# Optimization experiments

Measured on AMD Instinct MI355X. Metric: run time of the kernel, lower is better.

## Reference

```python
import jax, jax.numpy as jnp
import numpy as np

B = 8192
D = 512          # encode_length
H = 1024         # projection hidden
S = 4096         # fine_Nums (fine prototypes)
Y = 256          # coarse_num
GUMBEL_TEMP = 0.5
EPS_LOG = 1e-9
EPS_GUMBEL = 1e-20


def setup_inputs() -> dict:
    key = jax.random.key(0)
    ks = jax.random.split(key, 16)
    g = lambda k, shape, s: jax.random.normal(k, shape, dtype=jnp.float32) * s
    glorot = lambda k, shape: jax.random.uniform(k, shape, dtype=jnp.float32,
                                                 minval=-1.0, maxval=1.0) * jnp.sqrt(6.0 / (shape[0] + shape[1]))
    return {
        "X": jax.random.normal(ks[0], (B, D), dtype=jnp.float32),
        # projectionHead: Linear(D,H) -> ReLU -> Linear(H,D)
        "W1": g(ks[1], (D, H), 0.05), "b1": jnp.zeros((H,), jnp.float32),
        "W2": g(ks[2], (H, D), 0.05), "b2": jnp.zeros((D,), jnp.float32),
        # sigma_head: Linear(D,H) -> ReLU -> Linear(H,D)
        "Ws1": g(ks[3], (D, H), 0.05), "bs1": jnp.zeros((H,), jnp.float32),
        "Ws2": g(ks[4], (H, D), 0.05), "bs2": jnp.zeros((D,), jnp.float32),
        # prototype codebooks (glorot)
        "mu_y": glorot(ks[5], (Y, D)),
        "mu_s": glorot(ks[6], (S, D)),
        # reparameterization + gumbel noise (explicit for determinism)
        "eps": jax.random.normal(ks[7], (B, D), dtype=jnp.float32),
        "u_s": jax.random.uniform(ks[8], (B, S), dtype=jnp.float32),
        "u_y": jax.random.uniform(ks[9], (B, Y), dtype=jnp.float32),
    }


def _neg_sq_dist(x, c):
    # -||x_i - c_j||^2 computed via expansion (same math as (x-c)**2 sum)
    return -(jnp.sum(x * x, -1, keepdims=True)
             - 2.0 * x @ c.T
             + jnp.sum(c * c, -1)[None, :])


def _gumbel_softmax_soft(logits_original, u, temp):
    # torch: logits = log(softmax(logits_original) + 1e-9); y = softmax((logits + g)/temp)
    logits = jnp.log(jax.nn.softmax(logits_original, axis=-1) + EPS_LOG)
    gnoise = -jnp.log(-jnp.log(u + EPS_GUMBEL) + EPS_GUMBEL)
    return jax.nn.softmax((logits + gnoise) / temp, axis=-1)


def reference(X, W1, b1, W2, b2, Ws1, bs1, Ws2, bs2, mu_y, mu_s, eps, u_s, u_y):
    # VAE encode with reparameterization
    mu = jax.nn.relu(X @ W1 + b1) @ W2 + b2                    # [B, D]
    sigma = jax.nn.softplus(jax.nn.relu(X @ Ws1 + bs1) @ Ws2 + bs2)
    Z = mu + sigma * eps                                       # [B, D]

    # fine prototype routing: cdist + gumbel-softmax + hard assign
    logits_s = _neg_sq_dist(Z, mu_s)                            # [B, S]
    soft_prob = _gumbel_softmax_soft(logits_s, u_s, GUMBEL_TEMP)
    fine_idx = jnp.argmax(soft_prob, axis=1)                    # [B]
    hard_prob = jax.nn.one_hot(fine_idx, S, dtype=jnp.float32)  # [B, S]
    z_q = hard_prob @ mu_s                                      # selected fine proto [B, D]

    # coarse routing conditioned on Z and selected fine prototype
    logits_coarse = 0.5 * (_neg_sq_dist(Z, mu_y) + _neg_sq_dist(z_q, mu_y))  # [B, Y]
    soft_prob_y = _gumbel_softmax_soft(logits_coarse, u_y, GUMBEL_TEMP)
    batch_y = jnp.argmax(soft_prob_y, axis=1)                   # [B] int

    return mu, Z, soft_prob, soft_prob_y, hard_prob, batch_y
```

## Files before the change

### kernel.cpp

```cpp
#include <hip/hip_runtime.h>
#include <hip/hip_bf16.h>

#define B_ 8192
#define D_ 512
#define H_ 1024
#define S_ 4096
#define Y_ 256

constexpr size_t O_MU    = 0;
constexpr size_t O_Z     = (size_t)B_ * D_;
constexpr size_t O_SOFT  = O_Z + (size_t)B_ * D_;
constexpr size_t O_SOFTY = O_SOFT + (size_t)B_ * S_;
constexpr size_t O_HARD  = O_SOFTY + (size_t)B_ * Y_;
constexpr size_t O_BY    = O_HARD + (size_t)B_ * S_;

typedef _Float16 half8 __attribute__((ext_vector_type(8)));
typedef float f32x4 __attribute__((ext_vector_type(4)));
typedef unsigned int u32;

__device__ __forceinline__ void gload16(const void* g, void* l) {
  __builtin_amdgcn_global_load_lds((const __attribute__((address_space(1))) u32*)g,
                                   (__attribute__((address_space(3))) u32*)l,
                                   16, 0, 0);
}

__device__ __forceinline__ void split2(float x, _Float16& h, _Float16& l) {
  _Float16 hi = (_Float16)x;
  h = hi;
  l = (_Float16)((x - (float)hi) * 2048.0f);
}

__device__ __forceinline__ float blockMax(float v, float* sh) {
#pragma unroll
  for (int o = 32; o; o >>= 1) v = fmaxf(v, __shfl_xor(v, o));
  if ((threadIdx.x & 63) == 0) sh[threadIdx.x >> 6] = v;
  __syncthreads();
  float r = fmaxf(fmaxf(sh[0], sh[1]), fmaxf(sh[2], sh[3]));
  __syncthreads();
  return r;
}

__device__ __forceinline__ float blockSum(float v, float* sh) {
#pragma unroll
  for (int o = 32; o; o >>= 1) v += __shfl_xor(v, o);
  if ((threadIdx.x & 63) == 0) sh[threadIdx.x >> 6] = v;
  __syncthreads();
  float r = (sh[0] + sh[1]) + (sh[2] + sh[3]);
  __syncthreads();
  return r;
}

__device__ __forceinline__ void blockArgmax(float& v, int& i, float* shf, int* shi) {
#pragma unroll
  for (int o = 32; o; o >>= 1) {
    float v2 = __shfl_xor(v, o);
    int   i2 = __shfl_xor(i, o);
    if (v2 > v || (v2 == v && i2 < i)) { v = v2; i = i2; }
  }
  if ((threadIdx.x & 63) == 0) { shf[threadIdx.x >> 6] = v; shi[threadIdx.x >> 6] = i; }
  __syncthreads();
  float bv = shf[0]; int bi = shi[0];
#pragma unroll
  for (int k = 1; k < 4; ++k) {
    float v2 = shf[k]; int i2 = shi[k];
    if (v2 > bv || (v2 == bv && i2 < bi)) { bv = v2; bi = i2; }
  }
  v = bv; i = bi;
  __syncthreads();
}

__device__ void seg_split(const float* __restrict__ s, _Float16* __restrict__ h,
                          _Float16* __restrict__ l, size_t n, int b, int nb) {
  size_t i = (size_t)b * 256 + threadIdx.x;
  size_t st = (size_t)nb * 256;
  for (; i < n; i += st) { _Float16 hi, lo; split2(s[i], hi, lo); h[i] = hi; l[i] = lo; }
}

__device__ void seg_tsplit(const float* __restrict__ W, int K, int N,
                           _Float16* __restrict__ th, _Float16* __restrict__ tl,
                           int tile, float (*tl_lds)[33]) {
  int ntn = N / 32;
  int nb = (tile % ntn) * 32, kb = (tile / ntn) * 32;
  int tx = threadIdx.x & 31, ty = threadIdx.x >> 5;
  for (int r = ty; r < 32; r += 8)
    tl_lds[r][tx] = W[(size_t)(kb + r) * N + nb + tx];
  __syncthreads();
  for (int r = ty; r < 32; r += 8) {
    float x = tl_lds[tx][r];
    size_t o = (size_t)(nb + r) * K + kb + tx;
    _Float16 hi, lo; split2(x, hi, lo);
    th[o] = hi; tl[o] = lo;
  }
}

__device__ void seg_rownorm(const float* __restrict__ A, int K, float* __restrict__ out,
                            int tile) {
  int w = threadIdx.x >> 6, lane = threadIdx.x & 63;
  int row = tile * 4 + w;
  const float* a = A + (size_t)row * K;
  float s = 0.f;
  for (int k = lane; k < K; k += 64) { float x = a[k]; s += x * x; }
#pragma unroll
  for (int o = 32; o; o >>= 1) s += __shfl_xor(s, o);
  if (lane == 0) out[row] = s;
}

__global__ __launch_bounds__(256) void prep_kernel(
    const float* __restrict__ X, const float* __restrict__ W1, const float* __restrict__ Ws1,
    const float* __restrict__ W2, const float* __restrict__ Ws2,
    const float* __restrict__ mu_s, const float* __restrict__ mu_y,
    _Float16* XH, _Float16* XL, _Float16* MSH, _Float16* MSL,
    _Float16* MYH, _Float16* MYL,
    _Float16* W1CH, _Float16* W1CL, _Float16* W2CH, _Float16* W2CL,
    float* CS2, float* CY2) {
  __shared__ float tile[32][33];
  int b = blockIdx.x;
  if (b < 512)       seg_split(X,    XH,  XL,  (size_t)B_ * D_, b,        512);
  else if (b < 768)  seg_split(mu_s, MSH, MSL, (size_t)S_ * D_, b - 512,  256);
  else if (b < 784)  seg_split(mu_y, MYH, MYL, (size_t)Y_ * D_, b - 768,  16);
  else if (b < 1296) seg_tsplit(W1,  D_, H_, W1CH, W1CL, b - 784, tile);
  else if (b < 1808) seg_tsplit(Ws1, D_, H_, W1CH + (size_t)H_ * D_,
                                W1CL + (size_t)H_ * D_, b - 1296, tile);
  else if (b < 2320) seg_tsplit(W2,  H_, D_, W2CH, W2CL, b - 1808, tile);
  else if (b < 2832) seg_tsplit(Ws2, H_, D_, W2CH + (size_t)D_ * H_,
                                W2CL + (size_t)D_ * H_, b - 2320, tile);
  else if (b < 3856) seg_rownorm(mu_s, D_, CS2, b - 2832);
  else               seg_rownorm(mu_y, D_, CY2, b - 3856);
}

template <int EPI>
__launch_bounds__(256, 2)
__global__ void gemm_split(const _Float16* __restrict__ Ah, const _Float16* __restrict__ Al,
                           const _Float16* __restrict__ Bh, const _Float16* __restrict__ Bl,
                           int N, int K, int lda, int ldc, int nsplit, int aoff2,
                           const float* __restrict__ bias, const float* __restrict__ bias2,
                           float* __restrict__ Cf,
                           _Float16* __restrict__ Ch, _Float16* __restrict__ Cl,
                           const float* __restrict__ rown, const float* __restrict__ coln) {
  __shared__ _Float16 lds[4 * 8192];
  const int tid = threadIdx.x;
  const int w = tid >> 6, lane = tid & 63;
  const int m0 = blockIdx.y * 128, n0 = blockIdx.x * 128;
  const int g4 = lane >> 4, l15 = lane & 15;
  const int ln3 = lane >> 3, l7 = lane & 7;
  const int wsx = l7 ^ ln3;
  const int strideA = (w < 2) ? lda : K;
  const size_t laneoff = (size_t)ln3 * strideA + (size_t)wsx * 8;
  const int ashift = (n0 >= nsplit) ? aoff2 : 0;

  const _Float16* stage_src =
      (w == 0) ? (Ah + (size_t)m0 * lda + ashift) :
      (w == 1) ? (Al + (size_t)m0 * lda + ashift) :
      (w == 2) ? (Bh + (size_t)n0 * K) : (Bl + (size_t)n0 * K);
  _Float16* stage_dst = &lds[w * 8192];

  const int wm = w >> 1, wn = w & 1;

  f32x4 acc[4][4] = {};
  f32x4 accc[4][4] = {};

  for (int k0 = 0; k0 < K; k0 += 64) {
    const _Float16* sp = stage_src + k0 + laneoff;
#pragma unroll
    for (int q = 0; q < 16; ++q)
      gload16(sp + (size_t)q * 8 * strideA, stage_dst + q * 512);
    __syncthreads();

#pragma unroll
    for (int kk = 0; kk < 2; ++kk) {
      half8 ah[4], al[4], bh[4], bl[4];
#pragma unroll
      for (int mi = 0; mi < 4; ++mi) {
        int row = wm * 64 + mi * 16 + l15;
        int off = row * 64 + (((kk * 4 + g4) ^ (l15 & 7)) * 8);
        ah[mi] = *(const half8*)&lds[off];
        al[mi] = *(const half8*)&lds[8192 + off];
      }
#pragma unroll
      for (int ni = 0; ni < 4; ++ni) {
        int row = wn * 64 + ni * 16 + l15;
        int off = row * 64 + (((kk * 4 + g4) ^ (l15 & 7)) * 8);
        bh[ni] = *(const half8*)&lds[16384 + off];
        bl[ni] = *(const half8*)&lds[24576 + off];
      }
#pragma unroll
      for (int mi = 0; mi < 4; ++mi)
#pragma unroll
        for (int ni = 0; ni < 4; ++ni) {
          acc[mi][ni]  = __builtin_amdgcn_mfma_f32_16x16x32_f16(ah[mi], bh[ni], acc[mi][ni], 0, 0, 0);
          accc[mi][ni] = __builtin_amdgcn_mfma_f32_16x16x32_f16(ah[mi], bl[ni], accc[mi][ni], 0, 0, 0);
          accc[mi][ni] = __builtin_amdgcn_mfma_f32_16x16x32_f16(al[mi], bh[ni], accc[mi][ni], 0, 0, 0);
        }
    }
    __syncthreads();
  }

#pragma unroll
  for (int mi = 0; mi < 4; ++mi)
#pragma unroll
    for (int ni = 0; ni < 4; ++ni)
#pragma unroll
      for (int r = 0; r < 4; ++r) {
        int m = m0 + wm * 64 + mi * 16 + g4 * 4 + r;
        int n = n0 + wn * 64 + ni * 16 + l15;
        float c = acc[mi][ni][r] + accc[mi][ni][r] * (1.0f / 2048.0f);
        size_t idx = (size_t)m * ldc + n;
        if (EPI == 0) {
          float bv = (n < nsplit) ? bias[n] : bias2[n - nsplit];
          c = fmaxf(c + bv, 0.0f);
          _Float16 hi, lo; split2(c, hi, lo);
          Ch[idx] = hi; Cl[idx] = lo;
        } else if (EPI == 1) {
          float bv = (n < nsplit) ? bias[n] : bias2[n - nsplit];
          Cf[idx] = c + bv;
        } else {
          Cf[idx] = 2.0f * c - rown[m] - coln[n];
        }
      }
}

__global__ __launch_bounds__(256) void kz_kernel(const float* __restrict__ MPS,
                                                 const float* __restrict__ eps,
                                                 float* __restrict__ out,
                                                 _Float16* __restrict__ Zh,
                                                 _Float16* __restrict__ Zl,
                                                 float* __restrict__ z2) {
  __shared__ float sh[4];
  int row = blockIdx.x, t = threadIdx.x;
  float s = 0.f;
  for (int j = t; j < D_; j += 256) {
    size_t idx = (size_t)row * D_ + j;
    float m = MPS[(size_t)row * 1024 + j];
    float p = MPS[(size_t)row * 1024 + 512 + j];
    float e = eps[idx];
    float sp = fmaxf(p, 0.f) + log1pf(expf(-fabsf(p)));
    float z = m + sp * e;
    out[O_MU + idx] = m;
    out[O_Z + idx] = z;
    _Float16 hi, lo; split2(z, hi, lo);
    Zh[idx] = hi; Zl[idx] = lo;
    s += z * z;
  }
#pragma unroll
  for (int o = 32; o; o >>= 1) s += __shfl_xor(s, o);
  if ((t & 63) == 0) sh[t >> 6] = s;
  __syncthreads();
  if (t == 0) z2[row] = (sh[0] + sh[1]) + (sh[2] + sh[3]);
}

__global__ __launch_bounds__(256) void ks_kernel(const float* __restrict__ us,
                                                 const float* __restrict__ lzy,
                                                 const float* __restrict__ lsy,
                                                 const float* __restrict__ uy,
                                                 float* __restrict__ out) {
  __shared__ float shf[4];
  __shared__ int shi[4];
  int row = blockIdx.x, t = threadIdx.x;
  const float4* l4 = (const float4*)(out + O_SOFT + (size_t)row * S_) + t * 4;
  const float4* u4 = (const float4*)(us + (size_t)row * S_) + t * 4;

  float v[16];
#pragma unroll
  for (int q = 0; q < 4; ++q) {
    float4 x = l4[q];
    v[q * 4 + 0] = x.x; v[q * 4 + 1] = x.y; v[q * 4 + 2] = x.z; v[q * 4 + 3] = x.w;
  }
  float m1 = -3.4e38f;
#pragma unroll
  for (int k = 0; k < 16; ++k) m1 = fmaxf(m1, v[k]);
  m1 = blockMax(m1, shf);
  float s1 = 0.f;
#pragma unroll
  for (int k = 0; k < 16; ++k) { v[k] = __expf(v[k] - m1); s1 += v[k]; }
  s1 = blockSum(s1, shf);
  float is1 = 1.0f / s1;
  float m2 = -3.4e38f;
#pragma unroll
  for (int q = 0; q < 4; ++q) {
    float4 uu = u4[q];
    float ua[4] = {uu.x, uu.y, uu.z, uu.w};
#pragma unroll
    for (int e = 0; e < 4; ++e) {
      int k = q * 4 + e;
      float p = v[k] * is1 + 1e-9f;
      float g = -logf(-logf(ua[e] + 1e-20f) + 1e-20f);
      v[k] = (logf(p) + g) * 2.0f;
      m2 = fmaxf(m2, v[k]);
    }
  }
  m2 = blockMax(m2, shf);
  float s2 = 0.f;
#pragma unroll
  for (int k = 0; k < 16; ++k) { v[k] = __expf(v[k] - m2); s2 += v[k]; }
  s2 = blockSum(s2, shf);
  float is2 = 1.0f / s2;
  float bv = -3.4e38f; int bi = 0x7fffffff;
  float* so = out + O_SOFT + (size_t)row * S_ + (size_t)t * 16;
#pragma unroll
  for (int q = 0; q < 4; ++q) {
    float pe[4];
#pragma unroll
    for (int e = 0; e < 4; ++e) {
      int k = q * 4 + e;
      pe[e] = v[k] * is2;
      if (pe[e] > bv) { bv = pe[e]; bi = t * 16 + k; }
    }
    float4 pv; pv.x = pe[0]; pv.y = pe[1]; pv.z = pe[2]; pv.w = pe[3];
    ((float4*)so)[q] = pv;
  }
  blockArgmax(bv, bi, shf, shi);
  float* ho = out + O_HARD + (size_t)row * S_ + (size_t)t * 16;
#pragma unroll
  for (int q = 0; q < 4; ++q) {
    float4 hv;
    hv.x = (t * 16 + q * 4 + 0 == bi) ? 1.f : 0.f;
    hv.y = (t * 16 + q * 4 + 1 == bi) ? 1.f : 0.f;
    hv.z = (t * 16 + q * 4 + 2 == bi) ? 1.f : 0.f;
    hv.w = (t * 16 + q * 4 + 3 == bi) ? 1.f : 0.f;
    ((float4*)ho)[q] = hv;
  }

  float lc = 0.5f * (lzy[(size_t)row * Y_ + t] + lsy[(size_t)bi * Y_ + t]);
  float cm1 = blockMax(lc, shf);
  float ce = __expf(lc - cm1);
  float cs1 = blockSum(ce, shf);
  float cp = ce / cs1 + 1e-9f;
  float cg = -logf(-logf(uy[(size_t)row * Y_ + t] + 1e-20f) + 1e-20f);
  float ca = (logf(cp) + cg) * 2.0f;
  float cm2 = blockMax(ca, shf);
  float cy = __expf(ca - cm2);
  float cs2 = blockSum(cy, shf);
  float csp = cy / cs2;
  out[O_SOFTY + (size_t)row * Y_ + t] = csp;
  float cbv = csp; int cbi = t;
  blockArgmax(cbv, cbi, shf, shi);
  if (t == 0) out[O_BY + row] = (float)cbi;
}

extern "C" void kernel_launch(void* const* d_in, const int* in_sizes, int n_in,
                              void* d_out, int out_size, void* d_ws, size_t ws_size,
                              hipStream_t stream) {
  const float* X    = (const float*)d_in[0];
  const float* W1   = (const float*)d_in[1];
  const float* b1   = (const float*)d_in[2];
  const float* W2   = (const float*)d_in[3];
  const float* b2   = (const float*)d_in[4];
  const float* Ws1  = (const float*)d_in[5];
  const float* bs1  = (const float*)d_in[6];
  const float* Ws2  = (const float*)d_in[7];
  const float* bs2  = (const float*)d_in[8];
  const float* mu_y = (const float*)d_in[9];
  const float* mu_s = (const float*)d_in[10];
  const float* eps  = (const float*)d_in[11];
  const float* u_s  = (const float*)d_in[12];
  const float* u_y  = (const float*)d_in[13];
  float* out = (float*)d_out;

  char* ws = (char*)d_ws;
  _Float16* XH    = (_Float16*)(ws + 0);
  _Float16* XL    = (_Float16*)(ws + 8388608);
  _Float16* W1CH  = (_Float16*)(ws + 16777216);
  _Float16* W1CL  = (_Float16*)(ws + 18874368);
  _Float16* W2CH  = (_Float16*)(ws + 20971520);
  _Float16* W2CL  = (_Float16*)(ws + 23068672);
  _Float16* H1H   = (_Float16*)(ws + 25165824);
  _Float16* H1L   = (_Float16*)(ws + 58720256);
  float*    MPS   = (float*)  (ws + 92274688);
  float*    LZY   = (float*)  (ws + 0);
  float*    LSY   = (float*)  (ws + 8388608);
  const size_t RB = 125829120;
  _Float16* ZH   = (_Float16*)(ws + RB + 0);
  _Float16* MSH  = (_Float16*)(ws + RB + 8388608);
  _Float16* ZL   = (_Float16*)(ws + RB + 12582912);
  _Float16* MSL  = (_Float16*)(ws + RB + 20971520);
  _Float16* MYH  = (_Float16*)(ws + RB + 25165824);
  _Float16* MYL  = (_Float16*)(ws + RB + 25427968);
  float*    Z2   = (float*)  (ws + RB + 25690112);
  float*    CS2  = (float*)  (ws + RB + 25722880);
  float*    CY2  = (float*)  (ws + RB + 25739264);
  (void)ws_size; (void)in_sizes; (void)n_in; (void)out_size;

  float* LOGITS = out + O_SOFT;

  prep_kernel<<<3920, 256, 0, stream>>>(X, W1, Ws1, W2, Ws2, mu_s, mu_y,
                                        XH, XL, MSH, MSL, MYH, MYL,
                                        W1CH, W1CL, W2CH, W2CL, CS2, CY2);

  gemm_split<0><<<dim3(2 * H_ / 128, B_ / 128), 256, 0, stream>>>(
      XH, XL, W1CH, W1CL, 2 * H_, D_, D_, 2 * H_, H_, 0,
      b1, bs1, nullptr, H1H, H1L, nullptr, nullptr);

  gemm_split<1><<<dim3(2 * D_ / 128, B_ / 128), 256, 0, stream>>>(
      H1H, H1L, W2CH, W2CL, 2 * D_, H_, 2 * H_, 2 * D_, D_, H_,
      b2, bs2, MPS, nullptr, nullptr, nullptr, nullptr);

  kz_kernel<<<B_, 256, 0, stream>>>(MPS, eps, out, ZH, ZL, Z2);

  gemm_split<2><<<dim3(S_ / 128, B_ / 128), 256, 0, stream>>>(
      ZH, ZL, MSH, MSL, S_, D_, D_, S_, S_, 0,
      nullptr, nullptr, LOGITS, nullptr, nullptr, Z2, CS2);

  gemm_split<2><<<dim3(Y_ / 128, (B_ + S_) / 128), 256, 0, stream>>>(
      ZH, ZL, MYH, MYL, Y_, D_, D_, Y_, Y_, 0,
      nullptr, nullptr, LZY, nullptr, nullptr, Z2, CY2);

  ks_kernel<<<B_, 256, 0, stream>>>(u_s, LZY, LSY, u_y, out);
}
```

Baseline: 376.9 us.

## Fuse codebook prep into layer-1 GEMM and merge distance GEMMs into one launch

Moves the mu_s/mu_y fp16 splitting and row-norm computation out of the prep kernel and into extra blocks of the first-layer GEMM launch, so they run alongside it. Merges the fine and coarse distance GEMMs into a single kernel with a flattened block index. The GEMM body becomes a device function shared by these wrappers. The aim is fewer launches and less tail idle time; the cost is a mixed-work kernel whose auxiliary blocks reserve GEMM-sized LDS.

```diff
diff --git a/kernel.cpp b/kernel.cpp
--- a/kernel.cpp
+++ b/kernel.cpp
@@ -108,39 +108,31 @@
 __global__ __launch_bounds__(256) void prep_kernel(
     const float* __restrict__ X, const float* __restrict__ W1, const float* __restrict__ Ws1,
     const float* __restrict__ W2, const float* __restrict__ Ws2,
-    const float* __restrict__ mu_s, const float* __restrict__ mu_y,
-    _Float16* XH, _Float16* XL, _Float16* MSH, _Float16* MSL,
-    _Float16* MYH, _Float16* MYL,
-    _Float16* W1CH, _Float16* W1CL, _Float16* W2CH, _Float16* W2CL,
-    float* CS2, float* CY2) {
+    _Float16* XH, _Float16* XL,
+    _Float16* W1CH, _Float16* W1CL, _Float16* W2CH, _Float16* W2CL) {
   __shared__ float tile[32][33];
   int b = blockIdx.x;
-  if (b < 512)       seg_split(X,    XH,  XL,  (size_t)B_ * D_, b,        512);
-  else if (b < 768)  seg_split(mu_s, MSH, MSL, (size_t)S_ * D_, b - 512,  256);
-  else if (b < 784)  seg_split(mu_y, MYH, MYL, (size_t)Y_ * D_, b - 768,  16);
-  else if (b < 1296) seg_tsplit(W1,  D_, H_, W1CH, W1CL, b - 784, tile);
-  else if (b < 1808) seg_tsplit(Ws1, D_, H_, W1CH + (size_t)H_ * D_,
-                                W1CL + (size_t)H_ * D_, b - 1296, tile);
-  else if (b < 2320) seg_tsplit(W2,  H_, D_, W2CH, W2CL, b - 1808, tile);
-  else if (b < 2832) seg_tsplit(Ws2, H_, D_, W2CH + (size_t)D_ * H_,
-                                W2CL + (size_t)D_ * H_, b - 2320, tile);
-  else if (b < 3856) seg_rownorm(mu_s, D_, CS2, b - 2832);
-  else               seg_rownorm(mu_y, D_, CY2, b - 3856);
+  if (b < 512)       seg_split(X, XH, XL, (size_t)B_ * D_, b, 512);
+  else if (b < 1024) seg_tsplit(W1,  D_, H_, W1CH, W1CL, b - 512, tile);
+  else if (b < 1536) seg_tsplit(Ws1, D_, H_, W1CH + (size_t)H_ * D_,
+                                W1CL + (size_t)H_ * D_, b - 1024, tile);
+  else if (b < 2048) seg_tsplit(W2,  H_, D_, W2CH, W2CL, b - 1536, tile);
+  else               seg_tsplit(Ws2, H_, D_, W2CH + (size_t)D_ * H_,
+                                W2CL + (size_t)D_ * H_, b - 2048, tile);
 }
 
 template <int EPI>
-__launch_bounds__(256, 2)
-__global__ void gemm_split(const _Float16* __restrict__ Ah, const _Float16* __restrict__ Al,
-                           const _Float16* __restrict__ Bh, const _Float16* __restrict__ Bl,
-                           int N, int K, int lda, int ldc, int nsplit, int aoff2,
-                           const float* __restrict__ bias, const float* __restrict__ bias2,
-                           float* __restrict__ Cf,
-                           _Float16* __restrict__ Ch, _Float16* __restrict__ Cl,
-                           const float* __restrict__ rown, const float* __restrict__ coln) {
-  __shared__ _Float16 lds[4 * 8192];
+__device__ __forceinline__ void gemm_core(
+    _Float16* lds, int bx, int by,
+    const _Float16* __restrict__ Ah, const _Float16* __restrict__ Al,
+    const _Float16* __restrict__ Bh, const _Float16* __restrict__ Bl,
+    int N, int K, int lda, int ldc, int nsplit, int aoff2,
+    const float* __restrict__ bias, const float* __restrict__ bias2,
+    float* __restrict__ Cf, _Float16* __restrict__ Ch, _Float16* __restrict__ Cl,
+    const float* __restrict__ rown, const float* __restrict__ coln) {
   const int tid = threadIdx.x;
   const int w = tid >> 6, lane = tid & 63;
-  const int m0 = blockIdx.y * 128, n0 = blockIdx.x * 128;
+  const int m0 = by * 128, n0 = bx * 128;
   const int g4 = lane >> 4, l15 = lane & 15;
   const int ln3 = lane >> 3, l7 = lane & 7;
   const int wsx = l7 ^ ln3;
@@ -217,6 +209,64 @@
           Cf[idx] = 2.0f * c - rown[m] - coln[n];
         }
       }
+}
+
+__global__ __launch_bounds__(256, 2) void k_l1(
+    const _Float16* __restrict__ XH, const _Float16* __restrict__ XL,
+    const _Float16* __restrict__ W1CH, const _Float16* __restrict__ W1CL,
+    const float* __restrict__ b1, const float* __restrict__ bs1,
+    _Float16* H1H, _Float16* H1L,
+    const float* __restrict__ mu_s, const float* __restrict__ mu_y,
+    _Float16* MSH, _Float16* MSL, _Float16* MYH, _Float16* MYL,
+    float* CS2, float* CY2) {
+  __shared__ _Float16 lds[4 * 8192];
+  int b = blockIdx.x;
+  if (b < 1024) {
+    gemm_core<0>(lds, b & 15, b >> 4, XH, XL, W1CH, W1CL,
+                 2 * H_, D_, D_, 2 * H_, H_, 0, b1, bs1,
+                 nullptr, H1H, H1L, nullptr, nullptr);
+  } else {
+    float (*tile)[33] = (float(*)[33])lds;
+    int c = b - 1024;
+    if (c < 256)        seg_split(mu_s, MSH, MSL, (size_t)S_ * D_, c, 256);
+    else if (c < 272)   seg_split(mu_y, MYH, MYL, (size_t)Y_ * D_, c - 256, 16);
+    else if (c < 1296)  seg_rownorm(mu_s, D_, CS2, c - 272);
+    else                seg_rownorm(mu_y, D_, CY2, c - 1296);
+    (void)tile;
+  }
+}
+
+__global__ __launch_bounds__(256, 2) void k_l2(
+    const _Float16* __restrict__ H1H, const _Float16* __restrict__ H1L,
+    const _Float16* __restrict__ W2CH, const _Float16* __restrict__ W2CL,
+    const float* __restrict__ b2, const float* __restrict__ bs2,
+    float* MPS) {
+  __shared__ _Float16 lds[4 * 8192];
+  int b = blockIdx.x;
+  gemm_core<1>(lds, b & 7, b >> 3, H1H, H1L, W2CH, W2CL,
+               2 * D_, H_, 2 * H_, 2 * D_, D_, H_, b2, bs2,
+               MPS, nullptr, nullptr, nullptr, nullptr);
+}
+
+__global__ __launch_bounds__(256, 2) void k_dist(
+    const _Float16* __restrict__ ZH, const _Float16* __restrict__ ZL,
+    const _Float16* __restrict__ MSH, const _Float16* __restrict__ MSL,
+    const _Float16* __restrict__ MYH, const _Float16* __restrict__ MYL,
+    float* LOGITS, float* LZY,
+    const float* __restrict__ Z2, const float* __restrict__ CS2,
+    const float* __restrict__ CY2) {
+  __shared__ _Float16 lds[4 * 8192];
+  int b = blockIdx.x;
+  if (b < 2048) {
+    gemm_core<2>(lds, b & 31, b >> 5, ZH, ZL, MSH, MSL,
+                 S_, D_, D_, S_, 1 << 30, 0, nullptr, nullptr,
+                 LOGITS, nullptr, nullptr, Z2, CS2);
+  } else {
+    int c = b - 2048;
+    gemm_core<2>(lds, c & 1, c >> 1, ZH, ZL, MYH, MYL,
+                 Y_, D_, D_, Y_, 1 << 30, 0, nullptr, nullptr,
+                 LZY, nullptr, nullptr, Z2, CY2);
+  }
 }
 
 __global__ __launch_bounds__(256) void kz_kernel(const float* __restrict__ MPS,
@@ -367,7 +417,6 @@
   _Float16* H1L   = (_Float16*)(ws + 58720256);
   float*    MPS   = (float*)  (ws + 92274688);
   float*    LZY   = (float*)  (ws + 0);
-  float*    LSY   = (float*)  (ws + 8388608);
   const size_t RB = 125829120;
   _Float16* ZH   = (_Float16*)(ws + RB + 0);
   _Float16* MSH  = (_Float16*)(ws + RB + 8388608);
@@ -381,28 +430,20 @@
   (void)ws_size; (void)in_sizes; (void)n_in; (void)out_size;
 
   float* LOGITS = out + O_SOFT;
-
-  prep_kernel<<<3920, 256, 0, stream>>>(X, W1, Ws1, W2, Ws2, mu_s, mu_y,
-                                        XH, XL, MSH, MSL, MYH, MYL,
-                                        W1CH, W1CL, W2CH, W2CL, CS2, CY2);
-
-  gemm_split<0><<<dim3(2 * H_ / 128, B_ / 128), 256, 0, stream>>>(
-      XH, XL, W1CH, W1CL, 2 * H_, D_, D_, 2 * H_, H_, 0,
-      b1, bs1, nullptr, H1H, H1L, nullptr, nullptr);
-
-  gemm_split<1><<<dim3(2 * D_ / 128, B_ / 128), 256, 0, stream>>>(
-      H1H, H1L, W2CH, W2CL, 2 * D_, H_, 2 * H_, 2 * D_, D_, H_,
-      b2, bs2, MPS, nullptr, nullptr, nullptr, nullptr);
+  float* LSY = LZY + (size_t)B_ * Y_;
+
+  prep_kernel<<<2560, 256, 0, stream>>>(X, W1, Ws1, W2, Ws2,
+                                        XH, XL, W1CH, W1CL, W2CH, W2CL);
+
+  k_l1<<<2384, 256, 0, stream>>>(XH, XL, W1CH, W1CL, b1, bs1, H1H, H1L,
+                                 mu_s, mu_y, MSH, MSL, MYH, MYL, CS2, CY2);
+
+  k_l2<<<512, 256, 0, stream>>>(H1H, H1L, W2CH, W2CL, b2, bs2, MPS);
 
   kz_kernel<<<B_, 256, 0, stream>>>(MPS, eps, out, ZH, ZL, Z2);
 
-  gemm_split<2><<<dim3(S_ / 128, B_ / 128), 256, 0, stream>>>(
-      ZH, ZL, MSH, MSL, S_, D_, D_, S_, S_, 0,
-      nullptr, nullptr, LOGITS, nullptr, nullptr, Z2, CS2);
-
-  gemm_split<2><<<dim3(Y_ / 128, (B_ + S_) / 128), 256, 0, stream>>>(
-      ZH, ZL, MYH, MYL, Y_, D_, D_, Y_, Y_, 0,
-      nullptr, nullptr, LZY, nullptr, nullptr, Z2, CY2);
+  k_dist<<<2240, 256, 0, stream>>>(ZH, ZL, MSH, MSL, MYH, MYL,
+                                   LOGITS, LZY, Z2, CS2, CY2);
 
   ks_kernel<<<B_, 256, 0, stream>>>(u_s, LZY, LSY, u_y, out);
 }
```

Measured after the change: 378.7 us. No clear change (+0.5%).
